# Optimization experiments

Hardware: AMD Instinct MI355X
Metric: run time of the kernel (lower is better)

## Reference

```python
import jax, jax.numpy as jnp
import numpy as np

B = 4096      # number of snakes (graphs)
L = 256       # fixed snake length (nodes per chain)
N = B * L     # total nodes
HID = 32
OUT = 32
AUX = 32
FIN = 64
N_FRUITS = 1
AUX_IN = 2 + 1 + N_FRUITS * 2  # = 5


def _chain_edges():
    # chain edges i<->i+1 within each graph, both directions (PyG undirected chain)
    base = np.arange(L - 1)
    src1 = (np.arange(B)[:, None] * L + base[None, :]).ravel()
    dst1 = src1 + 1
    src = np.concatenate([src1, dst1])
    dst = np.concatenate([dst1, src1])
    return np.stack([src, dst]).astype(np.int64)  # [2, 2*(L-1)*B]


def setup_inputs() -> dict:
    key = jax.random.key(0)
    ks = jax.random.split(key, 16)

    def lin(k, fan_in, fan_out):
        k1, k2 = jax.random.split(k)
        bound = 1.0 / np.sqrt(fan_in)
        W = jax.random.uniform(k1, (fan_in, fan_out), jnp.float32, -bound, bound)
        b = jax.random.uniform(k2, (fan_out,), jnp.float32, -bound, bound)
        return W, b

    x = jax.random.normal(ks[0], (N, 2), jnp.float32)
    heads = jax.random.normal(ks[1], (B, 2), jnp.float32)
    body_sizes = jax.random.uniform(ks[2], (B, 1), jnp.float32)
    fruits = jax.random.normal(ks[3], (B, N_FRUITS, 2), jnp.float32)

    W1, b1 = lin(ks[4], 2, HID)
    W2, b2 = lin(ks[5], HID, HID)
    Wr, br = lin(ks[6], HID, OUT)
    Wa1, ba1 = lin(ks[7], AUX_IN, AUX)
    Wa2, ba2 = lin(ks[8], AUX, AUX)
    Wc, bc = lin(ks[9], OUT + AUX, FIN)
    Wp, bp = lin(ks[10], FIN, 5)
    Wv, bv = lin(ks[11], FIN, 1)

    edge_index = jnp.asarray(_chain_edges())
    batch_ids = jnp.repeat(jnp.arange(B, dtype=jnp.int64), L)

    return dict(x=x, heads=heads, body_sizes=body_sizes, fruits=fruits,
                W1=W1, b1=b1, W2=W2, b2=b2, Wr=Wr, br=br,
                Wa1=Wa1, ba1=ba1, Wa2=Wa2, ba2=ba2, Wc=Wc, bc=bc,
                Wp=Wp, bp=bp, Wv=Wv, bv=bv,
                edge_index=edge_index, batch_ids=batch_ids)


def _gcn_conv(h, W, b, src, dst):
    # PyG GCNConv: out = D^{-1/2} (A + I) D^{-1/2} (h W) + b, deg counts self-loop
    h = h @ W  # [N, F]
    ones = jnp.ones(src.shape[0], h.dtype)
    deg = jax.ops.segment_sum(ones, dst, num_segments=N) + 1.0  # self-loop
    dinv = jax.lax.rsqrt(deg)
    norm = dinv[src] * dinv[dst]  # [E]
    agg = jax.ops.segment_sum(norm[:, None] * h[src], dst, num_segments=N)
    agg = agg + (dinv * dinv)[:, None] * h  # self-loop messages
    return agg + b


def reference(x, heads, body_sizes, fruits,
              W1, b1, W2, b2, Wr, br, Wa1, ba1, Wa2, ba2,
              Wc, bc, Wp, bp, Wv, bv, edge_index, batch_ids):
    src, dst = edge_index[0], edge_index[1]
    h = jax.nn.relu(_gcn_conv(x, W1, b1, src, dst))
    h = jax.nn.relu(_gcn_conv(h, W2, b2, src, dst))
    # global mean pool per graph
    pooled = jax.ops.segment_sum(h, batch_ids, num_segments=B)
    counts = jax.ops.segment_sum(jnp.ones(N, h.dtype), batch_ids, num_segments=B)
    pooled = pooled / counts[:, None]
    body_emb = pooled @ Wr + br  # [B, OUT]

    aux_input = jnp.concatenate([heads, body_sizes,
                                 fruits.reshape(fruits.shape[0], -1)], axis=-1)
    aux = jax.nn.relu(aux_input @ Wa1 + ba1)
    aux = jax.nn.relu(aux @ Wa2 + ba2)

    combined = jnp.concatenate([body_emb, aux], axis=-1)
    combined = jax.nn.relu(combined @ Wc + bc)
    logits = combined @ Wp + bp  # [B, 5]
    value = combined @ Wv + bv   # [B, 1]
    return logits, value
```

## Files before the change

### kernel.cpp

```cpp
#include <hip/hip_runtime.h>


#define NB  4096
#define CL  256
#define HID 32
#define FIN 64

typedef __attribute__((ext_vector_type(8))) short bf16x8;
typedef __attribute__((ext_vector_type(4))) float f32x4;

__device__ __forceinline__ unsigned short f2bf(float f) {
    unsigned u = __builtin_bit_cast(unsigned, f);
    u += 0x7FFFu + ((u >> 16) & 1u);
    return (unsigned short)(u >> 16);
}
__device__ __forceinline__ float bf2f(unsigned short h) {
    unsigned u = ((unsigned)h) << 16;
    return __builtin_bit_cast(float, u);
}
__device__ __forceinline__ void gcn_coef(int n, float& nc, float& nl, float& nr) {
    const float IS3 = 0.57735026918962576f, IS2 = 0.70710678118654752f;
    const float dn = (n == 0 || n == CL - 1) ? IS2 : IS3;
    nc = dn * dn;
    nl = (n > 0)      ? dn * ((n == 1)      ? IS2 : IS3) : 0.0f;
    nr = (n < CL - 1) ? dn * ((n == CL - 2) ? IS2 : IS3) : 0.0f;
}

__global__ __launch_bounds__(256, 6) void snake_fused(
    const float* __restrict__ x,
    const float* __restrict__ heads,
    const float* __restrict__ body_sizes,
    const float* __restrict__ fruits,
    const float* __restrict__ W1, const float* __restrict__ b1,
    const float* __restrict__ W2, const float* __restrict__ b2,
    const float* __restrict__ Wr, const float* __restrict__ br,
    const float* __restrict__ Wa1, const float* __restrict__ ba1,
    const float* __restrict__ Wa2, const float* __restrict__ ba2,
    const float* __restrict__ Wc, const float* __restrict__ bc,
    const float* __restrict__ Wp, const float* __restrict__ bp,
    const float* __restrict__ Wv, const float* __restrict__ bv,
    float* __restrict__ out)
{
    __shared__ short Abuf[CL * 40];
    __shared__ float edgebuf[4][2][HID];
    __shared__ float waveparts[4][HID];

    const int b = blockIdx.x;
    const int i = threadIdx.x;
    const int w    = i >> 6;
    const int lane = i & 63;
    const int g    = lane >> 4;
    const int c    = lane & 15;

    bf16x8 Bh[2], Bl[2];
    #pragma unroll
    for (int nt = 0; nt < 2; ++nt) {
        #pragma unroll
        for (int j = 0; j < 8; ++j) {
            const float wv = W2[(8 * g + j) * HID + c + 16 * nt];
            const unsigned short h = f2bf(wv);
            Bh[nt][j] = (short)h;
            Bl[nt][j] = (short)f2bf(wv - bf2f(h));
        }
    }
    const float b2v0 = b2[c];
    const float b2v1 = b2[c + 16];

    float ncd, nld, nrd;
    gcn_coef(i, ncd, nld, nrd);
    const int il = (i > 0) ? i - 1 : i;
    const int ir = (i < CL - 1) ? i + 1 : i;
    float2* xb = reinterpret_cast<float2*>(Abuf);
    xb[i] = reinterpret_cast<const float2*>(x)[b * CL + i];
    __syncthreads();
    const float2 xc = xb[i];
    const float2 xl = xb[il];
    const float2 xr = xb[ir];
    __syncthreads();
    const float sxx = ncd * xc.x + nld * xl.x + nrd * xr.x;
    const float sxy = ncd * xc.y + nld * xl.y + nrd * xr.y;

    bf16x8 hv[4], lv[4];
    #pragma unroll
    for (int s = 0; s < 4; ++s) {
        #pragma unroll
        for (int j = 0; j < 8; ++j) {
            const int ch = 8 * s + j;
            const float r = fmaxf(fmaf(sxx, W1[ch], fmaf(sxy, W1[HID + ch], b1[ch])), 0.0f);
            const unsigned short h = f2bf(r);
            hv[s][j] = (short)h;
            lv[s][j] = (short)f2bf(r - bf2f(h));
        }
    }
    {
        bf16x8* ap = reinterpret_cast<bf16x8*>(&Abuf[i * 40]);
        #pragma unroll
        for (int s = 0; s < 4; ++s) ap[s] = hv[s];
    }
    __syncthreads();

    f32x4 acc[4][2];
    #pragma unroll
    for (int t = 0; t < 4; ++t) {
        #pragma unroll
        for (int nt = 0; nt < 2; ++nt) { f32x4 z = {0.f, 0.f, 0.f, 0.f}; acc[t][nt] = z; }
    }
    #pragma unroll
    for (int t = 0; t < 4; ++t) {
        const int node = 64 * w + 16 * t + c;
        const bf16x8 a = *reinterpret_cast<const bf16x8*>(&Abuf[node * 40 + 8 * g]);
        #pragma unroll
        for (int nt = 0; nt < 2; ++nt) {
            acc[t][nt] = __builtin_amdgcn_mfma_f32_16x16x32_bf16(a, Bh[nt], acc[t][nt], 0, 0, 0);
            acc[t][nt] = __builtin_amdgcn_mfma_f32_16x16x32_bf16(a, Bl[nt], acc[t][nt], 0, 0, 0);
        }
    }
    __syncthreads();
    {
        bf16x8* ap = reinterpret_cast<bf16x8*>(&Abuf[i * 40]);
        #pragma unroll
        for (int s = 0; s < 4; ++s) ap[s] = lv[s];
    }
    __syncthreads();
    #pragma unroll
    for (int t = 0; t < 4; ++t) {
        const int node = 64 * w + 16 * t + c;
        const bf16x8 a = *reinterpret_cast<const bf16x8*>(&Abuf[node * 40 + 8 * g]);
        #pragma unroll
        for (int nt = 0; nt < 2; ++nt)
            acc[t][nt] = __builtin_amdgcn_mfma_f32_16x16x32_bf16(a, Bh[nt], acc[t][nt], 0, 0, 0);
    }

    if (lane < 16) {
        edgebuf[w][0][c]      = acc[0][0][0];
        edgebuf[w][0][c + 16] = acc[0][1][0];
    } else if (lane >= 48) {
        edgebuf[w][1][c]      = acc[3][0][3];
        edgebuf[w][1][c + 16] = acc[3][1][3];
    }
    __syncthreads();

    float sum0 = 0.0f, sum1 = 0.0f;
    #pragma unroll
    for (int t = 0; t < 4; ++t) {
        const int nbase = 64 * w + 16 * t + 4 * g;
        float c0, l0, r0; gcn_coef(nbase + 0, c0, l0, r0);
        float c1, l1, r1; gcn_coef(nbase + 1, c1, l1, r1);
        float c2, l2, r2; gcn_coef(nbase + 2, c2, l2, r2);
        float c3, l3, r3; gcn_coef(nbase + 3, c3, l3, r3);
        #pragma unroll
        for (int nt = 0; nt < 2; ++nt) {
            const f32x4 v = acc[t][nt];
            const float Lsame = __shfl(acc[t][nt][3], lane - 16, 64);
            const float Lprev = __shfl(acc[(t > 0) ? t - 1 : 0][nt][3], c + 48, 64);
            float L = (g > 0) ? Lsame : Lprev;
            if (t == 0) {
                float eL = edgebuf[(w > 0) ? w - 1 : 0][1][c + 16 * nt];
                eL = (w > 0) ? eL : 0.0f;
                L = (g == 0) ? eL : L;
            }
            const float Rsame = __shfl(acc[t][nt][0], lane + 16, 64);
            const float Rnext = __shfl(acc[(t < 3) ? t + 1 : 3][nt][0], c, 64);
            float R = (g < 3) ? Rsame : Rnext;
            if (t == 3) {
                float eR = edgebuf[(w < 3) ? w + 1 : 3][0][c + 16 * nt];
                eR = (w < 3) ? eR : 0.0f;
                R = (g == 3) ? eR : R;
            }
            const float bb = (nt == 0) ? b2v0 : b2v1;
            const float h0 = fmaxf(c0 * v[0] + l0 * L    + r0 * v[1] + bb, 0.0f);
            const float h1 = fmaxf(c1 * v[1] + l1 * v[0] + r1 * v[2] + bb, 0.0f);
            const float h2 = fmaxf(c2 * v[2] + l2 * v[1] + r2 * v[3] + bb, 0.0f);
            const float h3 = fmaxf(c3 * v[3] + l3 * v[2] + r3 * R    + bb, 0.0f);
            const float hs = (h0 + h1) + (h2 + h3);
            if (nt == 0) sum0 += hs; else sum1 += hs;
        }
    }
    sum0 += __shfl_xor(sum0, 16, 64); sum0 += __shfl_xor(sum0, 32, 64);
    sum1 += __shfl_xor(sum1, 16, 64); sum1 += __shfl_xor(sum1, 32, 64);
    if (g == 0) { waveparts[w][c] = sum0; waveparts[w][c + 16] = sum1; }
    __syncthreads();

    if (i < 64) {
        const int kk = i & 31;
        const float pk_own = (waveparts[0][kk] + waveparts[1][kk] +
                              waveparts[2][kk] + waveparts[3][kk]) * (1.0f / 256.0f);
        float catv;
        if (i < HID) {
            float be = br[i];
            #pragma unroll 8
            for (int k = 0; k < HID; ++k)
                be = fmaf(__shfl(pk_own, k, 64), Wr[k * HID + i], be);
            catv = be;
        } else {
            const int cc = i - HID;
            float a = ba1[cc];
            a = fmaf(heads[2 * b],      Wa1[0 * HID + cc], a);
            a = fmaf(heads[2 * b + 1],  Wa1[1 * HID + cc], a);
            a = fmaf(body_sizes[b],     Wa1[2 * HID + cc], a);
            a = fmaf(fruits[2 * b],     Wa1[3 * HID + cc], a);
            a = fmaf(fruits[2 * b + 1], Wa1[4 * HID + cc], a);
            a = fmaxf(a, 0.0f);
            float a2 = ba2[cc];
            #pragma unroll 8
            for (int k = 0; k < HID; ++k)
                a2 = fmaf(__shfl(a, HID + k, 64), Wa2[k * HID + cc], a2);
            catv = fmaxf(a2, 0.0f);
        }
        float cb = bc[i];
        #pragma unroll 8
        for (int k = 0; k < FIN; ++k)
            cb = fmaf(__shfl(catv, k, 64), Wc[k * FIN + i], cb);
        cb = fmaxf(cb, 0.0f);
        float s0 = cb * Wp[i * 5 + 0];
        float s1 = cb * Wp[i * 5 + 1];
        float s2 = cb * Wp[i * 5 + 2];
        float s3 = cb * Wp[i * 5 + 3];
        float s4 = cb * Wp[i * 5 + 4];
        float s5 = cb * Wv[i];
        #pragma unroll
        for (int m = 1; m <= 32; m <<= 1) {
            s0 += __shfl_xor(s0, m, 64);
            s1 += __shfl_xor(s1, m, 64);
            s2 += __shfl_xor(s2, m, 64);
            s3 += __shfl_xor(s3, m, 64);
            s4 += __shfl_xor(s4, m, 64);
            s5 += __shfl_xor(s5, m, 64);
        }
        if (i == 0) {
            out[b * 5 + 0] = s0 + bp[0];
            out[b * 5 + 1] = s1 + bp[1];
            out[b * 5 + 2] = s2 + bp[2];
            out[b * 5 + 3] = s3 + bp[3];
            out[b * 5 + 4] = s4 + bp[4];
            out[NB * 5 + b] = s5 + bv[0];
        }
    }
}

extern "C" void kernel_launch(void* const* d_in, const int* in_sizes, int n_in,
                              void* d_out, int out_size, void* d_ws, size_t ws_size,
                              hipStream_t stream) {
    const float* x          = (const float*)d_in[0];
    const float* heads      = (const float*)d_in[1];
    const float* body_sizes = (const float*)d_in[2];
    const float* fruits     = (const float*)d_in[3];
    const float* W1 = (const float*)d_in[4];
    const float* b1 = (const float*)d_in[5];
    const float* W2 = (const float*)d_in[6];
    const float* b2 = (const float*)d_in[7];
    const float* Wr = (const float*)d_in[8];
    const float* br = (const float*)d_in[9];
    const float* Wa1 = (const float*)d_in[10];
    const float* ba1 = (const float*)d_in[11];
    const float* Wa2 = (const float*)d_in[12];
    const float* ba2 = (const float*)d_in[13];
    const float* Wc = (const float*)d_in[14];
    const float* bc = (const float*)d_in[15];
    const float* Wp = (const float*)d_in[16];
    const float* bp = (const float*)d_in[17];
    const float* Wv = (const float*)d_in[18];
    const float* bv = (const float*)d_in[19];

    float* out = (float*)d_out;
    snake_fused<<<NB, CL, 0, stream>>>(
        x, heads, body_sizes, fruits,
        W1, b1, W2, b2, Wr, br, Wa1, ba1, Wa2, ba2,
        Wc, bc, Wp, bp, Wv, bv, out);
}
```

Baseline: 141.6 us.

## Process four snakes per block, build MFMA operands in registers via shuffles

```diff
diff --git a/kernel.cpp b/kernel.cpp
--- a/kernel.cpp
+++ b/kernel.cpp
@@ -1,23 +1,25 @@
 #include <hip/hip_runtime.h>
+#include <hip/hip_bf16.h>
 
 
 #define NB  4096
 #define CL  256
 #define HID 32
 #define FIN 64
-
-typedef __attribute__((ext_vector_type(8))) short bf16x8;
-typedef __attribute__((ext_vector_type(4))) float f32x4;
-
-__device__ __forceinline__ unsigned short f2bf(float f) {
-    unsigned u = __builtin_bit_cast(unsigned, f);
-    u += 0x7FFFu + ((u >> 16) & 1u);
-    return (unsigned short)(u >> 16);
+#define SPB 4
+
+typedef __attribute__((ext_vector_type(8))) short    bf16x8;
+typedef __attribute__((ext_vector_type(4))) float    f32x4;
+typedef __attribute__((ext_vector_type(4))) unsigned u32x4;
+
+__device__ __forceinline__ unsigned pkbf(float a, float b) {
+    __hip_bfloat162 hb = __float22bfloat162_rn(make_float2(a, b));
+    unsigned u; __builtin_memcpy(&u, &hb, sizeof(u));
+    return u;
 }
-__device__ __forceinline__ float bf2f(unsigned short h) {
-    unsigned u = ((unsigned)h) << 16;
-    return __builtin_bit_cast(float, u);
-}
+__device__ __forceinline__ float bflo(unsigned u) { return __builtin_bit_cast(float, u << 16); }
+__device__ __forceinline__ float bfhi(unsigned u) { return __builtin_bit_cast(float, u & 0xffff0000u); }
+
 __device__ __forceinline__ void gcn_coef(int n, float& nc, float& nl, float& nr) {
     const float IS3 = 0.57735026918962576f, IS2 = 0.70710678118654752f;
     const float dn = (n == 0 || n == CL - 1) ? IS2 : IS3;
@@ -26,7 +28,7 @@
     nr = (n < CL - 1) ? dn * ((n == CL - 2) ? IS2 : IS3) : 0.0f;
 }
 
-__global__ __launch_bounds__(256, 6) void snake_fused(
+__global__ __launch_bounds__(256, 4) void snake_fused(
     const float* __restrict__ x,
     const float* __restrict__ heads,
     const float* __restrict__ body_sizes,
@@ -41,12 +43,14 @@
     const float* __restrict__ Wv, const float* __restrict__ bv,
     float* __restrict__ out)
 {
-    __shared__ short Abuf[CL * 40];
-    __shared__ float edgebuf[4][2][HID];
-    __shared__ float waveparts[4][HID];
-
-    const int b = blockIdx.x;
-    const int i = threadIdx.x;
+    __shared__ __align__(16) float edgebuf[SPB][4][2][HID];
+    __shared__ __align__(16) float waveparts[SPB][HID][4];
+    __shared__ __align__(16) float poolLDS[SPB][HID];
+    __shared__ __align__(16) float auxLDS[SPB][HID];
+    __shared__ __align__(16) float catLDS[SPB][FIN];
+
+    const int blk  = blockIdx.x;
+    const int i    = threadIdx.x;
     const int w    = i >> 6;
     const int lane = i & 63;
     const int g    = lane >> 4;
@@ -55,169 +59,205 @@
     bf16x8 Bh[2], Bl[2];
     #pragma unroll
     for (int nt = 0; nt < 2; ++nt) {
-        #pragma unroll
-        for (int j = 0; j < 8; ++j) {
-            const float wv = W2[(8 * g + j) * HID + c + 16 * nt];
-            const unsigned short h = f2bf(wv);
-            Bh[nt][j] = (short)h;
-            Bl[nt][j] = (short)f2bf(wv - bf2f(h));
-        }
-    }
-    const float b2v0 = b2[c];
-    const float b2v1 = b2[c + 16];
+        unsigned hh[4], ll[4];
+        #pragma unroll
+        for (int p = 0; p < 4; ++p) {
+            const float wa = W2[(8 * g + 2 * p)     * HID + c + 16 * nt];
+            const float wb = W2[(8 * g + 2 * p + 1) * HID + c + 16 * nt];
+            const unsigned hu = pkbf(wa, wb);
+            hh[p] = hu;
+            ll[p] = pkbf(wa - bflo(hu), wb - bfhi(hu));
+        }
+        u32x4 H = {hh[0], hh[1], hh[2], hh[3]};
+        u32x4 L = {ll[0], ll[1], ll[2], ll[3]};
+        Bh[nt] = __builtin_bit_cast(bf16x8, H);
+        Bl[nt] = __builtin_bit_cast(bf16x8, L);
+    }
+    const float b2v0 = b2[c], b2v1 = b2[c + 16];
+
+    const float4 W1a0 = *reinterpret_cast<const float4*>(W1 + 8 * g);
+    const float4 W1a1 = *reinterpret_cast<const float4*>(W1 + 8 * g + 4);
+    const float4 W1b0 = *reinterpret_cast<const float4*>(W1 + HID + 8 * g);
+    const float4 W1b1 = *reinterpret_cast<const float4*>(W1 + HID + 8 * g + 4);
+    const float4 b1v0 = *reinterpret_cast<const float4*>(b1 + 8 * g);
+    const float4 b1v1 = *reinterpret_cast<const float4*>(b1 + 8 * g + 4);
 
     float ncd, nld, nrd;
     gcn_coef(i, ncd, nld, nrd);
-    const int il = (i > 0) ? i - 1 : i;
-    const int ir = (i < CL - 1) ? i + 1 : i;
-    float2* xb = reinterpret_cast<float2*>(Abuf);
-    xb[i] = reinterpret_cast<const float2*>(x)[b * CL + i];
+
+    const float THIRD = 0.33333333333333333f;
+    const float I23   = 0.40824829046386302f;
+    const bool fixL = (w == 0) && (g == 0);
+    const bool fixR = (w == 3) && (g == 3);
+
+    #pragma unroll 1
+    for (int s = 0; s < SPB; ++s) {
+        const int gs = SPB * blk + s;
+        const float2* xs = reinterpret_cast<const float2*>(x) + gs * CL;
+
+        const float2 xc = xs[i];
+        const float2 xl = xs[i - (i > 0)];
+        const float2 xr = xs[i + (i < CL - 1)];
+        const float sxx = ncd * xc.x + nld * xl.x + nrd * xr.x;
+        const float sxy = ncd * xc.y + nld * xl.y + nrd * xr.y;
+
+        float sxA[4], syA[4];
+        #pragma unroll
+        for (int t = 0; t < 4; ++t) {
+            sxA[t] = __shfl(sxx, 16 * t + c, 64);
+            syA[t] = __shfl(sxy, 16 * t + c, 64);
+        }
+
+        f32x4 acc[4][2];
+        #pragma unroll
+        for (int t = 0; t < 4; ++t)
+            #pragma unroll
+            for (int nt = 0; nt < 2; ++nt) { f32x4 z = {0.f, 0.f, 0.f, 0.f}; acc[t][nt] = z; }
+
+        #pragma unroll
+        for (int t = 0; t < 4; ++t) {
+            const float sa = sxA[t], sb = syA[t];
+            const float r0 = fmaxf(fmaf(sa, W1a0.x, fmaf(sb, W1b0.x, b1v0.x)), 0.f);
+            const float r1 = fmaxf(fmaf(sa, W1a0.y, fmaf(sb, W1b0.y, b1v0.y)), 0.f);
+            const float r2 = fmaxf(fmaf(sa, W1a0.z, fmaf(sb, W1b0.z, b1v0.z)), 0.f);
+            const float r3 = fmaxf(fmaf(sa, W1a0.w, fmaf(sb, W1b0.w, b1v0.w)), 0.f);
+            const float r4 = fmaxf(fmaf(sa, W1a1.x, fmaf(sb, W1b1.x, b1v1.x)), 0.f);
+            const float r5 = fmaxf(fmaf(sa, W1a1.y, fmaf(sb, W1b1.y, b1v1.y)), 0.f);
+            const float r6 = fmaxf(fmaf(sa, W1a1.z, fmaf(sb, W1b1.z, b1v1.z)), 0.f);
+            const float r7 = fmaxf(fmaf(sa, W1a1.w, fmaf(sb, W1b1.w, b1v1.w)), 0.f);
+            const unsigned h0 = pkbf(r0, r1), h1 = pkbf(r2, r3);
+            const unsigned h2 = pkbf(r4, r5), h3 = pkbf(r6, r7);
+            const unsigned q0 = pkbf(r0 - bflo(h0), r1 - bfhi(h0));
+            const unsigned q1 = pkbf(r2 - bflo(h1), r3 - bfhi(h1));
+            const unsigned q2 = pkbf(r4 - bflo(h2), r5 - bfhi(h2));
+            const unsigned q3 = pkbf(r6 - bflo(h3), r7 - bfhi(h3));
+            u32x4 HU = {h0, h1, h2, h3};
+            u32x4 LU = {q0, q1, q2, q3};
+            const bf16x8 ah = __builtin_bit_cast(bf16x8, HU);
+            const bf16x8 al = __builtin_bit_cast(bf16x8, LU);
+            #pragma unroll
+            for (int nt = 0; nt < 2; ++nt) {
+                acc[t][nt] = __builtin_amdgcn_mfma_f32_16x16x32_bf16(ah, Bh[nt], acc[t][nt], 0, 0, 0);
+                acc[t][nt] = __builtin_amdgcn_mfma_f32_16x16x32_bf16(al, Bh[nt], acc[t][nt], 0, 0, 0);
+                acc[t][nt] = __builtin_amdgcn_mfma_f32_16x16x32_bf16(ah, Bl[nt], acc[t][nt], 0, 0, 0);
+            }
+        }
+
+        if (lane < 16) {
+            edgebuf[s][w][0][c]      = acc[0][0][0];
+            edgebuf[s][w][0][c + 16] = acc[0][1][0];
+        } else if (lane >= 48) {
+            edgebuf[s][w][1][c]      = acc[3][0][3];
+            edgebuf[s][w][1][c + 16] = acc[3][1][3];
+        }
+        __syncthreads();
+
+        float sum0 = 0.f, sum1 = 0.f;
+        #pragma unroll
+        for (int t = 0; t < 4; ++t) {
+            float c0 = THIRD, r0c = THIRD, l1c = THIRD;
+            float c3 = THIRD, l3c = THIRD, r2c = THIRD;
+            if (t == 0) { c0 = fixL ? 0.5f : THIRD; r0c = fixL ? I23 : THIRD; l1c = fixL ? I23 : THIRD; }
+            if (t == 3) { c3 = fixR ? 0.5f : THIRD; l3c = fixR ? I23 : THIRD; r2c = fixR ? I23 : THIRD; }
+            #pragma unroll
+            for (int nt = 0; nt < 2; ++nt) {
+                const f32x4 v = acc[t][nt];
+                const float Lsend = (g == 3) ? acc[(t > 0) ? t - 1 : 0][nt][3] : acc[t][nt][3];
+                const int   Lsrc  = (g == 0) ? (c + 48) : (lane - 16);
+                float L = __shfl(Lsend, Lsrc, 64);
+                if (t == 0) {
+                    float eL = edgebuf[s][(w > 0) ? w - 1 : 0][1][c + 16 * nt];
+                    eL = (w > 0) ? eL : 0.f;
+                    L = (g == 0) ? eL : L;
+                }
+                const float Rsend = (g == 0) ? acc[(t < 3) ? t + 1 : 3][nt][0] : acc[t][nt][0];
+                const int   Rsrc  = (g == 3) ? c : (lane + 16);
+                float R = __shfl(Rsend, Rsrc, 64);
+                if (t == 3) {
+                    float eR = edgebuf[s][(w < 3) ? w + 1 : 3][0][c + 16 * nt];
+                    eR = (w < 3) ? eR : 0.f;
+                    R = (g == 3) ? eR : R;
+                }
+                const float bb = (nt == 0) ? b2v0 : b2v1;
+                const float h0 = fmaxf(fmaf(c0,    v[0], fmaf(THIRD, L,    fmaf(r0c,  v[1], bb))), 0.f);
+                const float h1 = fmaxf(fmaf(THIRD, v[1], fmaf(l1c,   v[0], fmaf(THIRD, v[2], bb))), 0.f);
+                const float h2 = fmaxf(fmaf(THIRD, v[2], fmaf(THIRD, v[1], fmaf(r2c,  v[3], bb))), 0.f);
+                const float h3 = fmaxf(fmaf(c3,    v[3], fmaf(l3c,   v[2], fmaf(THIRD, R,   bb))), 0.f);
+                const float hs = (h0 + h1) + (h2 + h3);
+                if (nt == 0) sum0 += hs; else sum1 += hs;
+            }
+        }
+        sum0 += __shfl_xor(sum0, 16, 64); sum0 += __shfl_xor(sum0, 32, 64);
+        sum1 += __shfl_xor(sum1, 16, 64); sum1 += __shfl_xor(sum1, 32, 64);
+        if (g == 0) {
+            waveparts[s][c][w]      = sum0;
+            waveparts[s][c + 16][w] = sum1;
+        }
+    }
     __syncthreads();
-    const float2 xc = xb[i];
-    const float2 xl = xb[il];
-    const float2 xr = xb[ir];
+
+    const int gsH = SPB * blk + w;
+    if (lane < HID) {
+        const f32x4 wp = *reinterpret_cast<const f32x4*>(&waveparts[w][lane][0]);
+        poolLDS[w][lane] = (wp.x + wp.y + wp.z + wp.w) * (1.0f / CL);
+    } else {
+        const int cc = lane - HID;
+        float a = ba1[cc];
+        a = fmaf(heads[2 * gsH],      Wa1[0 * HID + cc], a);
+        a = fmaf(heads[2 * gsH + 1],  Wa1[1 * HID + cc], a);
+        a = fmaf(body_sizes[gsH],     Wa1[2 * HID + cc], a);
+        a = fmaf(fruits[2 * gsH],     Wa1[3 * HID + cc], a);
+        a = fmaf(fruits[2 * gsH + 1], Wa1[4 * HID + cc], a);
+        auxLDS[w][cc] = fmaxf(a, 0.f);
+    }
     __syncthreads();
-    const float sxx = ncd * xc.x + nld * xl.x + nrd * xr.x;
-    const float sxy = ncd * xc.y + nld * xl.y + nrd * xr.y;
-
-    bf16x8 hv[4], lv[4];
-    #pragma unroll
-    for (int s = 0; s < 4; ++s) {
-        #pragma unroll
-        for (int j = 0; j < 8; ++j) {
-            const int ch = 8 * s + j;
-            const float r = fmaxf(fmaf(sxx, W1[ch], fmaf(sxy, W1[HID + ch], b1[ch])), 0.0f);
-            const unsigned short h = f2bf(r);
-            hv[s][j] = (short)h;
-            lv[s][j] = (short)f2bf(r - bf2f(h));
-        }
-    }
+
+    if (lane < HID) {
+        float be0 = br[lane], be1 = 0.f;
+        const float4* p4 = reinterpret_cast<const float4*>(poolLDS[w]);
+        #pragma unroll
+        for (int k4 = 0; k4 < 8; ++k4) {
+            const float4 p = p4[k4];
+            be0 = fmaf(p.x, Wr[(4 * k4 + 0) * HID + lane], be0);
+            be1 = fmaf(p.y, Wr[(4 * k4 + 1) * HID + lane], be1);
+            be0 = fmaf(p.z, Wr[(4 * k4 + 2) * HID + lane], be0);
+            be1 = fmaf(p.w, Wr[(4 * k4 + 3) * HID + lane], be1);
+        }
+        catLDS[w][lane] = be0 + be1;
+    } else {
+        const int cc = lane - HID;
+        float a0 = ba2[cc], a1 = 0.f;
+        const float4* p4 = reinterpret_cast<const float4*>(auxLDS[w]);
+        #pragma unroll
+        for (int k4 = 0; k4 < 8; ++k4) {
+            const float4 p = p4[k4];
+            a0 = fmaf(p.x, Wa2[(4 * k4 + 0) * HID + cc], a0);
+            a1 = fmaf(p.y, Wa2[(4 * k4 + 1) * HID + cc], a1);
+            a0 = fmaf(p.z, Wa2[(4 * k4 + 2) * HID + cc], a0);
+            a1 = fmaf(p.w, Wa2[(4 * k4 + 3) * HID + cc], a1);
+        }
+        catLDS[w][lane] = fmaxf(a0 + a1, 0.f);
+    }
+    __syncthreads();
+
     {
-        bf16x8* ap = reinterpret_cast<bf16x8*>(&Abuf[i * 40]);
-        #pragma unroll
-        for (int s = 0; s < 4; ++s) ap[s] = hv[s];
-    }
-    __syncthreads();
-
-    f32x4 acc[4][2];
-    #pragma unroll
-    for (int t = 0; t < 4; ++t) {
-        #pragma unroll
-        for (int nt = 0; nt < 2; ++nt) { f32x4 z = {0.f, 0.f, 0.f, 0.f}; acc[t][nt] = z; }
-    }
-    #pragma unroll
-    for (int t = 0; t < 4; ++t) {
-        const int node = 64 * w + 16 * t + c;
-        const bf16x8 a = *reinterpret_cast<const bf16x8*>(&Abuf[node * 40 + 8 * g]);
-        #pragma unroll
-        for (int nt = 0; nt < 2; ++nt) {
-            acc[t][nt] = __builtin_amdgcn_mfma_f32_16x16x32_bf16(a, Bh[nt], acc[t][nt], 0, 0, 0);
-            acc[t][nt] = __builtin_amdgcn_mfma_f32_16x16x32_bf16(a, Bl[nt], acc[t][nt], 0, 0, 0);
-        }
-    }
-    __syncthreads();
-    {
-        bf16x8* ap = reinterpret_cast<bf16x8*>(&Abuf[i * 40]);
-        #pragma unroll
-        for (int s = 0; s < 4; ++s) ap[s] = lv[s];
-    }
-    __syncthreads();
-    #pragma unroll
-    for (int t = 0; t < 4; ++t) {
-        const int node = 64 * w + 16 * t + c;
-        const bf16x8 a = *reinterpret_cast<const bf16x8*>(&Abuf[node * 40 + 8 * g]);
-        #pragma unroll
-        for (int nt = 0; nt < 2; ++nt)
-            acc[t][nt] = __builtin_amdgcn_mfma_f32_16x16x32_bf16(a, Bh[nt], acc[t][nt], 0, 0, 0);
-    }
-
-    if (lane < 16) {
-        edgebuf[w][0][c]      = acc[0][0][0];
-        edgebuf[w][0][c + 16] = acc[0][1][0];
-    } else if (lane >= 48) {
-        edgebuf[w][1][c]      = acc[3][0][3];
-        edgebuf[w][1][c + 16] = acc[3][1][3];
-    }
-    __syncthreads();
-
-    float sum0 = 0.0f, sum1 = 0.0f;
-    #pragma unroll
-    for (int t = 0; t < 4; ++t) {
-        const int nbase = 64 * w + 16 * t + 4 * g;
-        float c0, l0, r0; gcn_coef(nbase + 0, c0, l0, r0);
-        float c1, l1, r1; gcn_coef(nbase + 1, c1, l1, r1);
-        float c2, l2, r2; gcn_coef(nbase + 2, c2, l2, r2);
-        float c3, l3, r3; gcn_coef(nbase + 3, c3, l3, r3);
-        #pragma unroll
-        for (int nt = 0; nt < 2; ++nt) {
-            const f32x4 v = acc[t][nt];
-            const float Lsame = __shfl(acc[t][nt][3], lane - 16, 64);
-            const float Lprev = __shfl(acc[(t > 0) ? t - 1 : 0][nt][3], c + 48, 64);
-            float L = (g > 0) ? Lsame : Lprev;
-            if (t == 0) {
-                float eL = edgebuf[(w > 0) ? w - 1 : 0][1][c + 16 * nt];
-                eL = (w > 0) ? eL : 0.0f;
-                L = (g == 0) ? eL : L;
-            }
-            const float Rsame = __shfl(acc[t][nt][0], lane + 16, 64);
-            const float Rnext = __shfl(acc[(t < 3) ? t + 1 : 3][nt][0], c, 64);
-            float R = (g < 3) ? Rsame : Rnext;
-            if (t == 3) {
-                float eR = edgebuf[(w < 3) ? w + 1 : 3][0][c + 16 * nt];
-                eR = (w < 3) ? eR : 0.0f;
-                R = (g == 3) ? eR : R;
-            }
-            const float bb = (nt == 0) ? b2v0 : b2v1;
-            const float h0 = fmaxf(c0 * v[0] + l0 * L    + r0 * v[1] + bb, 0.0f);
-            const float h1 = fmaxf(c1 * v[1] + l1 * v[0] + r1 * v[2] + bb, 0.0f);
-            const float h2 = fmaxf(c2 * v[2] + l2 * v[1] + r2 * v[3] + bb, 0.0f);
-            const float h3 = fmaxf(c3 * v[3] + l3 * v[2] + r3 * R    + bb, 0.0f);
-            const float hs = (h0 + h1) + (h2 + h3);
-            if (nt == 0) sum0 += hs; else sum1 += hs;
-        }
-    }
-    sum0 += __shfl_xor(sum0, 16, 64); sum0 += __shfl_xor(sum0, 32, 64);
-    sum1 += __shfl_xor(sum1, 16, 64); sum1 += __shfl_xor(sum1, 32, 64);
-    if (g == 0) { waveparts[w][c] = sum0; waveparts[w][c + 16] = sum1; }
-    __syncthreads();
-
-    if (i < 64) {
-        const int kk = i & 31;
-        const float pk_own = (waveparts[0][kk] + waveparts[1][kk] +
-                              waveparts[2][kk] + waveparts[3][kk]) * (1.0f / 256.0f);
-        float catv;
-        if (i < HID) {
-            float be = br[i];
-            #pragma unroll 8
-            for (int k = 0; k < HID; ++k)
-                be = fmaf(__shfl(pk_own, k, 64), Wr[k * HID + i], be);
-            catv = be;
-        } else {
-            const int cc = i - HID;
-            float a = ba1[cc];
-            a = fmaf(heads[2 * b],      Wa1[0 * HID + cc], a);
-            a = fmaf(heads[2 * b + 1],  Wa1[1 * HID + cc], a);
-            a = fmaf(body_sizes[b],     Wa1[2 * HID + cc], a);
-            a = fmaf(fruits[2 * b],     Wa1[3 * HID + cc], a);
-            a = fmaf(fruits[2 * b + 1], Wa1[4 * HID + cc], a);
-            a = fmaxf(a, 0.0f);
-            float a2 = ba2[cc];
-            #pragma unroll 8
-            for (int k = 0; k < HID; ++k)
-                a2 = fmaf(__shfl(a, HID + k, 64), Wa2[k * HID + cc], a2);
-            catv = fmaxf(a2, 0.0f);
-        }
-        float cb = bc[i];
-        #pragma unroll 8
-        for (int k = 0; k < FIN; ++k)
-            cb = fmaf(__shfl(catv, k, 64), Wc[k * FIN + i], cb);
-        cb = fmaxf(cb, 0.0f);
-        float s0 = cb * Wp[i * 5 + 0];
-        float s1 = cb * Wp[i * 5 + 1];
-        float s2 = cb * Wp[i * 5 + 2];
-        float s3 = cb * Wp[i * 5 + 3];
-        float s4 = cb * Wp[i * 5 + 4];
-        float s5 = cb * Wv[i];
+        float cb0 = bc[lane], cb1 = 0.f;
+        const float4* c4p = reinterpret_cast<const float4*>(catLDS[w]);
+        #pragma unroll
+        for (int k4 = 0; k4 < 16; ++k4) {
+            const float4 p = c4p[k4];
+            cb0 = fmaf(p.x, Wc[(4 * k4 + 0) * FIN + lane], cb0);
+            cb1 = fmaf(p.y, Wc[(4 * k4 + 1) * FIN + lane], cb1);
+            cb0 = fmaf(p.z, Wc[(4 * k4 + 2) * FIN + lane], cb0);
+            cb1 = fmaf(p.w, Wc[(4 * k4 + 3) * FIN + lane], cb1);
+        }
+        const float cb = fmaxf(cb0 + cb1, 0.f);
+        float s0 = cb * Wp[lane * 5 + 0];
+        float s1 = cb * Wp[lane * 5 + 1];
+        float s2 = cb * Wp[lane * 5 + 2];
+        float s3 = cb * Wp[lane * 5 + 3];
+        float s4 = cb * Wp[lane * 5 + 4];
+        float s5 = cb * Wv[lane];
         #pragma unroll
         for (int m = 1; m <= 32; m <<= 1) {
             s0 += __shfl_xor(s0, m, 64);
@@ -227,13 +267,13 @@
             s4 += __shfl_xor(s4, m, 64);
             s5 += __shfl_xor(s5, m, 64);
         }
-        if (i == 0) {
-            out[b * 5 + 0] = s0 + bp[0];
-            out[b * 5 + 1] = s1 + bp[1];
-            out[b * 5 + 2] = s2 + bp[2];
-            out[b * 5 + 3] = s3 + bp[3];
-            out[b * 5 + 4] = s4 + bp[4];
-            out[NB * 5 + b] = s5 + bv[0];
+        if (lane == 0) {
+            out[gsH * 5 + 0] = s0 + bp[0];
+            out[gsH * 5 + 1] = s1 + bp[1];
+            out[gsH * 5 + 2] = s2 + bp[2];
+            out[gsH * 5 + 3] = s3 + bp[3];
+            out[gsH * 5 + 4] = s4 + bp[4];
+            out[NB * 5 + gsH] = s5 + bv[0];
         }
     }
 }
@@ -263,7 +303,7 @@
     const float* bv = (const float*)d_in[19];
 
     float* out = (float*)d_out;
-    snake_fused<<<NB, CL, 0, stream>>>(
+    snake_fused<<<NB / SPB, CL, 0, stream>>>(
         x, heads, body_sizes, fruits,
         W1, b1, W2, b2, Wr, br, Wa1, ba1, Wa2, ba2,
         Wc, bc, Wp, bp, Wv, bv, out);
```

Result: faster. 126.8 us (-10.5%).
